# Kernel optimization log

Hardware: AMD Instinct MI355X
Metric: run time of the kernel (lower is better)

The kernel has to match this reference:

```python
import jax, jax.numpy as jnp
import numpy as np

WSCALE = 0.05  # keep ReLU MLP activations in a sane range


def setup_inputs() -> dict:
    key = jax.random.key(0)
    ks = jax.random.split(key, 9)
    B, D, H = 2048, 64, 512
    return {
        "x": jax.random.normal(ks[0], (B, D), dtype=jnp.float32),
        "W1": jax.random.normal(ks[1], (H, D), dtype=jnp.float32) * WSCALE,
        "b1": jax.random.normal(ks[2], (H,), dtype=jnp.float32) * WSCALE,
        "W2": jax.random.normal(ks[3], (H, H), dtype=jnp.float32) * WSCALE,
        "b2": jax.random.normal(ks[4], (H,), dtype=jnp.float32) * WSCALE,
        "W3": jax.random.normal(ks[5], (H, H), dtype=jnp.float32) * WSCALE,
        "b3": jax.random.normal(ks[6], (H,), dtype=jnp.float32) * WSCALE,
        "W4": jax.random.normal(ks[7], (D, H), dtype=jnp.float32) * WSCALE,
        "b4": jax.random.normal(ks[8], (D,), dtype=jnp.float32) * WSCALE,
    }


def reference(x, W1, b1, W2, b2, W3, b3, W4, b4):
    # Score network: ReLU MLP (weights stored PyTorch-style [out, in]).
    a1 = x @ W1.T + b1          # [B, H]
    h1 = jax.nn.relu(a1)
    a2 = h1 @ W2.T + b2
    h2 = jax.nn.relu(a2)
    a3 = h2 @ W3.T + b3
    h3 = jax.nn.relu(a3)
    s = h3 @ W4.T + b4          # [B, D] score

    # Divergence = trace of Jacobian ds/dx per sample.
    # Per-sample J = W4 @ diag(m3) @ W3 @ diag(m2) @ W2 @ diag(m1) @ W1,
    # with m_k = 1[a_k > 0] (ReLU derivative; 0 at 0 like torch autograd).
    m1 = (a1 > 0).astype(x.dtype)
    m2 = (a2 > 0).astype(x.dtype)
    m3 = (a3 > 0).astype(x.dtype)
    T = m1[:, :, None] * W1[None, :, :]                 # [B, H, D]
    T = m2[:, :, None] * jnp.einsum('ij,bjd->bid', W2, T)  # [B, H, D]
    T = m3[:, :, None] * jnp.einsum('ij,bjd->bid', W3, T)  # [B, H, D]
    div = jnp.einsum('dj,bjd->b', W4, T)                # trace of J, [B]

    # Hyvarinen score: 0.5 * ||s||^2 + div
    val = 0.5 * jnp.sum(s * s, axis=1) + div
    return val
```

## Files before the change

kernel.cpp:

```cpp
#include <hip/hip_runtime.h>
#include <stdint.h>


typedef __attribute__((ext_vector_type(8))) short short8;
typedef __attribute__((ext_vector_type(4))) float f32x4;

union U16x8 {
  uint4 u;
  short8 s;
};

__device__ __forceinline__ uint16_t f2bf(float f) {
  uint32_t u = __float_as_uint(f);
  uint32_t lsb = (u >> 16) & 1u;
  u += 0x7FFFu + lsb;
  return (uint16_t)(u >> 16);
}

__device__ __forceinline__ void lds_load16(const uint4* gsrc, uint4* ldst) {
  __builtin_amdgcn_global_load_lds(
      (const __attribute__((address_space(1))) void*)gsrc,
      (__attribute__((address_space(3))) void*)ldst, 16, 0, 0);
}

__global__ __launch_bounds__(256) void convert_kernel(
    const float* __restrict__ W1, const float* __restrict__ W2,
    const float* __restrict__ W3, const float* __restrict__ W4,
    uint16_t* __restrict__ A2swz, uint16_t* __restrict__ A3swz,
    uint16_t* __restrict__ B1swz, uint16_t* __restrict__ B4swz,
    float* __restrict__ W2Tf, float* __restrict__ W3Tf,
    float* __restrict__ W1Tf, float* __restrict__ W4Tf) {
  const int i = blockIdx.x * 256 + threadIdx.x;
  if (i < 262144) {
    const int e = i;
    const int f = e >> 3, j = e & 7;
    const int lane = f & 63, fk = f >> 6;
    const int kc = fk & 15, r16 = fk >> 4;
    const int l15 = lane & 15, quad = lane >> 4;
    const int row = r16 * 16 + l15, col = kc * 32 + quad * 8 + j;
    A2swz[e] = f2bf(W2[row * 512 + col]);
  } else if (i < 524288) {
    const int e = i - 262144;
    const int f = e >> 3, j = e & 7;
    const int lane = f & 63, fk = f >> 6;
    const int kc = fk & 15, r16 = fk >> 4;
    const int l15 = lane & 15, quad = lane >> 4;
    const int row = r16 * 16 + l15, col = kc * 32 + quad * 8 + j;
    A3swz[e] = f2bf(W3[col * 512 + row]);
  } else if (i < 557056) {
    const int e = i - 524288;
    const int f = e >> 3, j = e & 7;
    const int lane = f & 63, fk = f >> 6;
    const int kc = fk >> 2, jt = fk & 3;
    const int l15 = lane & 15, quad = lane >> 4;
    const int d = jt * 16 + l15, col = kc * 32 + quad * 8 + j;
    B1swz[e] = f2bf(W1[col * 64 + d]);
  } else if (i < 589824) {
    const int e = i - 557056;
    const int f = e >> 3, j = e & 7;
    const int lane = f & 63, fk = f >> 6;
    const int kc = fk >> 2, jt = fk & 3;
    const int l15 = lane & 15, quad = lane >> 4;
    const int d = jt * 16 + l15, col = kc * 32 + quad * 8 + j;
    B4swz[e] = f2bf(W4[d * 512 + col]);
  } else if (i < 851968) {
    const int e = i - 589824;
    const int k = e >> 9, jj = e & 511;
    W2Tf[e] = W2[jj * 512 + k];
  } else if (i < 1114112) {
    const int e = i - 851968;
    const int k = e >> 9, jj = e & 511;
    W3Tf[e] = W3[jj * 512 + k];
  } else if (i < 1146880) {
    const int e = i - 1114112;
    const int k = e >> 9, jj = e & 511;
    W1Tf[e] = W1[jj * 64 + k];
  } else if (i < 1179648) {
    const int e = i - 1146880;
    const int k = e >> 6, d = e & 63;
    W4Tf[e] = W4[d * 512 + k];
  }
}

__device__ __forceinline__ void relu_store_mask4(
    float acc[4], float (*hdst)[4], uint32_t* __restrict__ mbase,
    int t, int lane, int wv) {
#pragma unroll
  for (int s = 0; s < 4; ++s) {
    const unsigned long long bal = __ballot(acc[s] > 0.f);
    if (lane == 0) {
      uint2 w2;
      w2.x = (uint32_t)bal;
      w2.y = (uint32_t)(bal >> 32);
      *(uint2*)(mbase + (size_t)s * 16 + 2 * wv) = w2;
    }
  }
  float4 r;
  r.x = acc[0] > 0.f ? acc[0] : 0.f;
  r.y = acc[1] > 0.f ? acc[1] : 0.f;
  r.z = acc[2] > 0.f ? acc[2] : 0.f;
  r.w = acc[3] > 0.f ? acc[3] : 0.f;
  *(float4*)&hdst[t][0] = r;
}

__device__ __forceinline__ void fwd_layer(
    const float* __restrict__ WT, const float* __restrict__ bias,
    const float (* __restrict__ src)[4], float (* __restrict__ dst)[4],
    uint32_t* __restrict__ mbase, int t, int lane, int wv, int K) {
  float acc[4];
  {
    const float bj = bias[t];
    acc[0] = bj; acc[1] = bj; acc[2] = bj; acc[3] = bj;
  }
  const float* Wp = WT + t;
  float wA[8], wB[8];
#pragma unroll
  for (int j = 0; j < 8; ++j) wA[j] = Wp[(size_t)j * 512];
#pragma unroll 1
  for (int kb = 0; kb < K; kb += 16) {
#pragma unroll
    for (int j = 0; j < 8; ++j) wB[j] = Wp[(size_t)(kb + 8 + j) * 512];
#pragma unroll
    for (int j = 0; j < 8; ++j) {
      const float4 h = *(const float4*)&src[kb + j][0];
      const float w = wA[j];
      acc[0] = fmaf(w, h.x, acc[0]); acc[1] = fmaf(w, h.y, acc[1]);
      acc[2] = fmaf(w, h.z, acc[2]); acc[3] = fmaf(w, h.w, acc[3]);
    }
    if (kb + 16 < K) {
#pragma unroll
      for (int j = 0; j < 8; ++j) wA[j] = Wp[(size_t)(kb + 16 + j) * 512];
    }
#pragma unroll
    for (int j = 0; j < 8; ++j) {
      const float4 h = *(const float4*)&src[kb + 8 + j][0];
      const float w = wB[j];
      acc[0] = fmaf(w, h.x, acc[0]); acc[1] = fmaf(w, h.y, acc[1]);
      acc[2] = fmaf(w, h.z, acc[2]); acc[3] = fmaf(w, h.w, acc[3]);
    }
  }
  relu_store_mask4(acc, dst, mbase, t, lane, wv);
}

__global__ __launch_bounds__(512) void forward_kernel(
    const float* __restrict__ x,
    const float* __restrict__ W1Tf, const float* __restrict__ b1,
    const float* __restrict__ W2Tf, const float* __restrict__ b2,
    const float* __restrict__ W3Tf, const float* __restrict__ b3,
    const float* __restrict__ W4Tf, const float* __restrict__ b4,
    uint32_t* __restrict__ m1p, uint32_t* __restrict__ m2p,
    uint32_t* __restrict__ m3p, float* __restrict__ out) {
  __shared__ float xs[64][4];
  __shared__ float hA[512][4];
  __shared__ float hB[512][4];
  __shared__ float p4[4][2][64];
  const int t = threadIdx.x;
  const int lane = t & 63, wv = t >> 6;
  const int b0 = blockIdx.x * 4;

  if (t < 256) {
    const int k = t >> 2, s = t & 3;
    xs[k][s] = x[(size_t)(b0 + s) * 64 + k];
  }
  __syncthreads();

  fwd_layer(W1Tf, b1, xs, hA, m1p + (size_t)b0 * 16, t, lane, wv, 64);
  __syncthreads();
  fwd_layer(W2Tf, b2, hA, hB, m2p + (size_t)b0 * 16, t, lane, wv, 512);
  __syncthreads();
  fwd_layer(W3Tf, b3, hB, hA, m3p + (size_t)b0 * 16, t, lane, wv, 512);
  __syncthreads();

  {
    const int s = wv & 3, hh = wv >> 2, d = lane;
    const int k0 = hh * 256;
    const float* Wp = W4Tf + (size_t)k0 * 64 + d;
    float ap[4] = {0.f, 0.f, 0.f, 0.f};
    float wA[8], wB[8];
#pragma unroll
    for (int j = 0; j < 8; ++j) wA[j] = Wp[(size_t)j * 64];
#pragma unroll 1
    for (int kb = 0; kb < 256; kb += 16) {
#pragma unroll
      for (int j = 0; j < 8; ++j) wB[j] = Wp[(size_t)(kb + 8 + j) * 64];
#pragma unroll
      for (int j = 0; j < 8; ++j)
        ap[j & 3] = fmaf(wA[j], hA[k0 + kb + j][s], ap[j & 3]);
      if (kb + 16 < 256) {
#pragma unroll
        for (int j = 0; j < 8; ++j) wA[j] = Wp[(size_t)(kb + 16 + j) * 64];
      }
#pragma unroll
      for (int j = 0; j < 8; ++j)
        ap[j & 3] = fmaf(wB[j], hA[k0 + kb + 8 + j][s], ap[j & 3]);
    }
    p4[s][hh][d] = (ap[0] + ap[1]) + (ap[2] + ap[3]);
  }
  __syncthreads();
  if (wv < 4) {
    const int s = wv, d = lane;
    const float a4 = p4[s][0][d] + p4[s][1][d] + b4[d];
    float sq = a4 * a4;
#pragma unroll
    for (int off = 32; off; off >>= 1) sq += __shfl_down(sq, off, 64);
    if (lane == 0) out[b0 + s] = 0.5f * sq;
  }
}

__device__ __forceinline__ void expand_mask(uint32_t byte8, uint32_t mk[4]) {
#pragma unroll
  for (int i = 0; i < 4; ++i) {
    mk[i] = (((byte8 >> (2 * i)) & 1u) ? 0x0000FFFFu : 0u) |
            (((byte8 >> (2 * i + 1)) & 1u) ? 0xFFFF0000u : 0u);
  }
}

__global__ __launch_bounds__(512, 4) void div_kernel(
    const uint4* __restrict__ A2swz, const uint4* __restrict__ A3swz,
    const uint4* __restrict__ B1swz, const uint4* __restrict__ B4swz,
    const uint32_t* __restrict__ m1p, const uint32_t* __restrict__ m2p,
    const uint32_t* __restrict__ m3p, float* __restrict__ out) {
  __shared__ uint4 sfrag[3][16][64];
  __shared__ uint4 emask[8][16][4];
  const int t = threadIdx.x;
  const int lane = t & 63, wv = t >> 6;
  const int quad = lane >> 4, l15 = lane & 15;
  const int g4 = blockIdx.x;
  const int rowB0 = blockIdx.y * 64;
  const int sLoc = wv & 3;
  const int b = g4 * 4 + sLoc;
  const int r16b = blockIdx.y * 4;
  const bool isC = (wv < 4);

  const uint4* sb = (wv < 2) ? A2swz : (wv < 4) ? B1swz : (wv < 6) ? A3swz : B4swz;

  f32x4 acc[4][4];
#pragma unroll
  for (int it = 0; it < 4; ++it)
#pragma unroll
    for (int jt = 0; jt < 4; ++jt) acc[it][jt] = (f32x4){0.f, 0.f, 0.f, 0.f};

  {
    const uint32_t* mp = (isC ? m1p : m3p) + (size_t)b * 16;
    const int kcl = lane >> 2, qd = lane & 3;
    const uint32_t word = mp[kcl];
    uint32_t mk[4];
    expand_mask((word >> (qd * 8)) & 0xFFu, mk);
    uint4 v;
    v.x = mk[0]; v.y = mk[1]; v.z = mk[2]; v.w = mk[3];
    emask[wv][kcl][qd] = v;
  }

  auto stage = [&](int sbuf, int kc) {
#pragma unroll
    for (int q = 0; q < 2; ++q) {
      const int sub = (wv & 1) * 2 + q;
      const size_t off = ((wv & 2) == 0)
          ? ((size_t)((r16b + sub) * 16 + kc) * 64 + lane)
          : ((size_t)(kc * 4 + sub) * 64 + lane);
      lds_load16(sb + off, &sfrag[sbuf][wv * 2 + q][0]);
    }
  };

  stage(0, 0);
  stage(1, 1);
  __builtin_amdgcn_sched_barrier(0);
  asm volatile("s_waitcnt vmcnt(2)" ::: "memory");
  __builtin_amdgcn_s_barrier();
  __builtin_amdgcn_sched_barrier(0);

  const int base = isC ? 0 : 8;

#pragma unroll 1
  for (int kc = 0; kc < 16; ++kc) {
    const int rb = kc % 3;
    if (kc < 14) stage((kc + 2) % 3, kc + 2);

    const uint4 mku = emask[wv][kc][quad];

    uint4 a[4], u[4];
#pragma unroll
    for (int q = 0; q < 4; ++q) {
      a[q] = sfrag[rb][base + q][lane];
      u[q] = sfrag[rb][base + 4 + q][lane];
    }

    short8 bf[4];
#pragma unroll
    for (int jt = 0; jt < 4; ++jt) {
      U16x8 uu;
      uu.u = u[jt];
      uu.u.x &= mku.x; uu.u.y &= mku.y; uu.u.z &= mku.z; uu.u.w &= mku.w;
      bf[jt] = uu.s;
    }
#pragma unroll
    for (int it = 0; it < 4; ++it) {
      U16x8 ua;
      ua.u = a[it];
      const short8 af = ua.s;
#pragma unroll
      for (int jt = 0; jt < 4; ++jt)
        acc[it][jt] = __builtin_amdgcn_mfma_f32_16x16x32_bf16(af, bf[jt], acc[it][jt], 0, 0, 0);
    }

    if (kc < 14) {
      asm volatile("s_waitcnt vmcnt(2)" ::: "memory");
    } else if (kc == 14) {
      asm volatile("s_waitcnt vmcnt(0)" ::: "memory");
    }
    if (kc < 15) {
      __builtin_amdgcn_s_barrier();
      __builtin_amdgcn_sched_barrier(0);
    }
  }

  __syncthreads();
  float* cxf = (float*)&sfrag[0][0][0];
  float dsum = 0.f;
  const uint32_t* m2w = m2p + (size_t)b * 16;
#pragma unroll
  for (int h = 0; h < 2; ++h) {
    if (isC) {
#pragma unroll
      for (int ith = 0; ith < 2; ++ith)
#pragma unroll
        for (int jt = 0; jt < 4; ++jt) {
          float* crow = &cxf[((size_t)sLoc * 32 + ith * 16 + quad * 4) * 65 +
                             jt * 16 + l15];
          crow[0 * 65] = acc[h * 2 + ith][jt][0];
          crow[1 * 65] = acc[h * 2 + ith][jt][1];
          crow[2 * 65] = acc[h * 2 + ith][jt][2];
          crow[3 * 65] = acc[h * 2 + ith][jt][3];
        }
    }
    __syncthreads();
    if (!isC) {
#pragma unroll
      for (int ith = 0; ith < 2; ++ith) {
        const int it = h * 2 + ith;
        const int rloc = it * 16 + quad * 4;
        const uint32_t md = m2w[(rowB0 + rloc) >> 5];
        const uint32_t bits = (md >> (rloc & 31)) & 0xFu;
        const float w0 = (bits & 1u) ? 1.f : 0.f;
        const float w1 = (bits & 2u) ? 1.f : 0.f;
        const float w2 = (bits & 4u) ? 1.f : 0.f;
        const float w3 = (bits & 8u) ? 1.f : 0.f;
#pragma unroll
        for (int jt = 0; jt < 4; ++jt) {
          const float* crow = &cxf[((size_t)sLoc * 32 + ith * 16 + quad * 4) * 65 +
                                   jt * 16 + l15];
          dsum = fmaf(w0, acc[it][jt][0] * crow[0 * 65], dsum);
          dsum = fmaf(w1, acc[it][jt][1] * crow[1 * 65], dsum);
          dsum = fmaf(w2, acc[it][jt][2] * crow[2 * 65], dsum);
          dsum = fmaf(w3, acc[it][jt][3] * crow[3 * 65], dsum);
        }
      }
    }
    __syncthreads();
  }
  if (!isC) {
#pragma unroll
    for (int off = 32; off; off >>= 1) dsum += __shfl_down(dsum, off, 64);
    if (lane == 0) atomicAdd(out + b, dsum);
  }
}

extern "C" void kernel_launch(void* const* d_in, const int* in_sizes, int n_in,
                              void* d_out, int out_size, void* d_ws, size_t ws_size,
                              hipStream_t stream) {
  const float* x  = (const float*)d_in[0];
  const float* W1 = (const float*)d_in[1];
  const float* b1 = (const float*)d_in[2];
  const float* W2 = (const float*)d_in[3];
  const float* b2 = (const float*)d_in[4];
  const float* W3 = (const float*)d_in[5];
  const float* b3 = (const float*)d_in[6];
  const float* W4 = (const float*)d_in[7];
  const float* b4 = (const float*)d_in[8];
  float* out = (float*)d_out;

  char* ws = (char*)d_ws;
  uint16_t* A2swz = (uint16_t*)(ws + 0);
  uint16_t* A3swz = (uint16_t*)(ws + 524288);
  uint16_t* B1swz = (uint16_t*)(ws + 1048576);
  uint16_t* B4swz = (uint16_t*)(ws + 1114112);
  float*    W2Tf  = (float*)(ws + 1179648);
  float*    W3Tf  = (float*)(ws + 2228224);
  float*    W1Tf  = (float*)(ws + 3276800);
  float*    W4Tf  = (float*)(ws + 3407872);
  uint32_t* m1p   = (uint32_t*)(ws + 3538944);
  uint32_t* m2p   = (uint32_t*)(ws + 3670016);
  uint32_t* m3p   = (uint32_t*)(ws + 3801088);
  if (ws_size < 3932160) return;

  convert_kernel<<<4608, 256, 0, stream>>>(W1, W2, W3, W4,
                                           A2swz, A3swz, B1swz, B4swz,
                                           W2Tf, W3Tf, W1Tf, W4Tf);
  forward_kernel<<<512, 512, 0, stream>>>(x, W1Tf, b1, W2Tf, b2, W3Tf, b3,
                                          W4Tf, b4, m1p, m2p, m3p, out);
  div_kernel<<<dim3(512, 8), 512, 0, stream>>>((const uint4*)A2swz,
                                               (const uint4*)A3swz,
                                               (const uint4*)B1swz,
                                               (const uint4*)B4swz,
                                               m1p, m2p, m3p, out);
}
```

Before: 266.0 us.

## Load masked B fragments straight to registers, stage only A through LDS

Each wave now loads its B operand fragments (B1 or B4) from global memory directly into registers, prefetched one k-chunk ahead. Only the A operand (A2 or A3) still goes through the triple-buffered LDS ring, with one async load per wave instead of two. This halves the per-iteration LDS reads and shrinks the async staging work. In exchange, each wave fetches B on its own rather than sharing it through LDS, which adds redundant global/L2 traffic and register pressure. The vmcnt waits are adjusted to match the new number of outstanding loads.

Result: slower. 271.7 us (+2.1%).

```diff
diff --git a/kernel.cpp b/kernel.cpp
--- a/kernel.cpp
+++ b/kernel.cpp
@@ -232,7 +232,8 @@
   const int r16b = blockIdx.y * 4;
   const bool isC = (wv < 4);
 
-  const uint4* sb = (wv < 2) ? A2swz : (wv < 4) ? B1swz : (wv < 6) ? A3swz : B4swz;
+  const uint4* sbA = isC ? A2swz : A3swz;
+  const uint4* sbB = isC ? B1swz : B4swz;
 
   f32x4 acc[4][4];
 #pragma unroll
@@ -251,48 +252,48 @@
     emask[wv][kcl][qd] = v;
   }
 
-  auto stage = [&](int sbuf, int kc) {
-#pragma unroll
-    for (int q = 0; q < 2; ++q) {
-      const int sub = (wv & 1) * 2 + q;
-      const size_t off = ((wv & 2) == 0)
-          ? ((size_t)((r16b + sub) * 16 + kc) * 64 + lane)
-          : ((size_t)(kc * 4 + sub) * 64 + lane);
-      lds_load16(sb + off, &sfrag[sbuf][wv * 2 + q][0]);
-    }
+  auto stageA = [&](int sbuf, int kc) {
+    const size_t off = (size_t)((r16b + (wv & 3)) * 16 + kc) * 64 + lane;
+    lds_load16(sbA + off, &sfrag[sbuf][wv][0]);
   };
 
-  stage(0, 0);
-  stage(1, 1);
+  uint4 bfr[4];
+  stageA(0, 0);
+#pragma unroll
+  for (int jt = 0; jt < 4; ++jt) bfr[jt] = sbB[(size_t)jt * 64 + lane];
+  stageA(1, 1);
   __builtin_amdgcn_sched_barrier(0);
-  asm volatile("s_waitcnt vmcnt(2)" ::: "memory");
+  asm volatile("s_waitcnt vmcnt(1)" ::: "memory");
   __builtin_amdgcn_s_barrier();
   __builtin_amdgcn_sched_barrier(0);
 
-  const int base = isC ? 0 : 8;
+  const int base = isC ? 0 : 4;
 
 #pragma unroll 1
   for (int kc = 0; kc < 16; ++kc) {
     const int rb = kc % 3;
-    if (kc < 14) stage((kc + 2) % 3, kc + 2);
 
     const uint4 mku = emask[wv][kc][quad];
-
-    uint4 a[4], u[4];
-#pragma unroll
-    for (int q = 0; q < 4; ++q) {
-      a[q] = sfrag[rb][base + q][lane];
-      u[q] = sfrag[rb][base + 4 + q][lane];
-    }
 
     short8 bf[4];
 #pragma unroll
     for (int jt = 0; jt < 4; ++jt) {
       U16x8 uu;
-      uu.u = u[jt];
+      uu.u = bfr[jt];
       uu.u.x &= mku.x; uu.u.y &= mku.y; uu.u.z &= mku.z; uu.u.w &= mku.w;
       bf[jt] = uu.s;
     }
+    if (kc < 15) {
+#pragma unroll
+      for (int jt = 0; jt < 4; ++jt)
+        bfr[jt] = sbB[(size_t)((kc + 1) * 4 + jt) * 64 + lane];
+    }
+    if (kc < 14) stageA((kc + 2) % 3, kc + 2);
+
+    uint4 a[4];
+#pragma unroll
+    for (int q = 0; q < 4; ++q) a[q] = sfrag[rb][base + q][lane];
+
 #pragma unroll
     for (int it = 0; it < 4; ++it) {
       U16x8 ua;
@@ -304,7 +305,7 @@
     }
 
     if (kc < 14) {
-      asm volatile("s_waitcnt vmcnt(2)" ::: "memory");
+      asm volatile("s_waitcnt vmcnt(1)" ::: "memory");
     } else if (kc == 14) {
       asm volatile("s_waitcnt vmcnt(0)" ::: "memory");
     }
```

## Repartition divergence kernel waves by row tile instead of sample

Applied to the files above, without the earlier changes.

Each wave now owns one 16-row A tile and loops over the 4 samples in the block, applying each sample's mask to the A fragment instead of the B fragment. Before, each wave handled one sample and loaded all 4 A tiles. This cuts per-wave LDS reads of A fragments from 4 to 1 per k-step while keeping the MFMA count the same. The cost is 4 mask reads and ANDs per step, plus 4 reductions and 4 atomics per wave at the end. The first barrier now also waits for LDS counter zero so the mask table is visible.

Result: slower. 273.4 us (+2.8%).

```diff
diff --git a/kernel.cpp b/kernel.cpp
--- a/kernel.cpp
+++ b/kernel.cpp
@@ -221,86 +221,88 @@
     const uint32_t* __restrict__ m1p, const uint32_t* __restrict__ m2p,
     const uint32_t* __restrict__ m3p, float* __restrict__ out) {
   __shared__ uint4 sfrag[3][16][64];
-  __shared__ uint4 emask[8][16][4];
+  __shared__ uint4 emask2[2][4][16][4];
   const int t = threadIdx.x;
   const int lane = t & 63, wv = t >> 6;
   const int quad = lane >> 4, l15 = lane & 15;
   const int g4 = blockIdx.x;
   const int rowB0 = blockIdx.y * 64;
-  const int sLoc = wv & 3;
-  const int b = g4 * 4 + sLoc;
+  const int q = wv & 3;
   const int r16b = blockIdx.y * 4;
   const bool isC = (wv < 4);
+  const int role = isC ? 0 : 1;
 
   const uint4* sb = (wv < 2) ? A2swz : (wv < 4) ? B1swz : (wv < 6) ? A3swz : B4swz;
 
   f32x4 acc[4][4];
 #pragma unroll
-  for (int it = 0; it < 4; ++it)
-#pragma unroll
-    for (int jt = 0; jt < 4; ++jt) acc[it][jt] = (f32x4){0.f, 0.f, 0.f, 0.f};
+  for (int s = 0; s < 4; ++s)
+#pragma unroll
+    for (int jt = 0; jt < 4; ++jt) acc[s][jt] = (f32x4){0.f, 0.f, 0.f, 0.f};
 
   {
-    const uint32_t* mp = (isC ? m1p : m3p) + (size_t)b * 16;
+    const int r = wv >> 2, s = wv & 3;
+    const uint32_t* mp = (r == 0 ? m1p : m3p) + (size_t)(g4 * 4 + s) * 16;
     const int kcl = lane >> 2, qd = lane & 3;
     const uint32_t word = mp[kcl];
     uint32_t mk[4];
     expand_mask((word >> (qd * 8)) & 0xFFu, mk);
     uint4 v;
     v.x = mk[0]; v.y = mk[1]; v.z = mk[2]; v.w = mk[3];
-    emask[wv][kcl][qd] = v;
+    emask2[r][s][kcl][qd] = v;
   }
 
   auto stage = [&](int sbuf, int kc) {
 #pragma unroll
-    for (int q = 0; q < 2; ++q) {
-      const int sub = (wv & 1) * 2 + q;
+    for (int qq = 0; qq < 2; ++qq) {
+      const int sub = (wv & 1) * 2 + qq;
       const size_t off = ((wv & 2) == 0)
           ? ((size_t)((r16b + sub) * 16 + kc) * 64 + lane)
           : ((size_t)(kc * 4 + sub) * 64 + lane);
-      lds_load16(sb + off, &sfrag[sbuf][wv * 2 + q][0]);
+      lds_load16(sb + off, &sfrag[sbuf][wv * 2 + qq][0]);
     }
   };
 
   stage(0, 0);
   stage(1, 1);
   __builtin_amdgcn_sched_barrier(0);
-  asm volatile("s_waitcnt vmcnt(2)" ::: "memory");
+  asm volatile("s_waitcnt vmcnt(2) lgkmcnt(0)" ::: "memory");
   __builtin_amdgcn_s_barrier();
   __builtin_amdgcn_sched_barrier(0);
 
-  const int base = isC ? 0 : 8;
+  const int abase = isC ? 0 : 8;
+  const int ubase = isC ? 4 : 12;
 
 #pragma unroll 1
   for (int kc = 0; kc < 16; ++kc) {
     const int rb = kc % 3;
     if (kc < 14) stage((kc + 2) % 3, kc + 2);
 
-    const uint4 mku = emask[wv][kc][quad];
-
-    uint4 a[4], u[4];
-#pragma unroll
-    for (int q = 0; q < 4; ++q) {
-      a[q] = sfrag[rb][base + q][lane];
-      u[q] = sfrag[rb][base + 4 + q][lane];
-    }
-
-    short8 bf[4];
+    const uint4 a1 = sfrag[rb][abase + q][lane];
+    uint4 u[4];
+#pragma unroll
+    for (int jt = 0; jt < 4; ++jt) u[jt] = sfrag[rb][ubase + jt][lane];
+
+    short8 bu[4];
 #pragma unroll
     for (int jt = 0; jt < 4; ++jt) {
       U16x8 uu;
       uu.u = u[jt];
-      uu.u.x &= mku.x; uu.u.y &= mku.y; uu.u.z &= mku.z; uu.u.w &= mku.w;
-      bf[jt] = uu.s;
-    }
-#pragma unroll
-    for (int it = 0; it < 4; ++it) {
-      U16x8 ua;
-      ua.u = a[it];
-      const short8 af = ua.s;
+      bu[jt] = uu.s;
+    }
+
+#pragma unroll
+    for (int s = 0; s < 4; ++s) {
+      const uint4 mku = emask2[role][s][kc][quad];
+      U16x8 am;
+      am.u.x = a1.x & mku.x;
+      am.u.y = a1.y & mku.y;
+      am.u.z = a1.z & mku.z;
+      am.u.w = a1.w & mku.w;
+      const short8 af = am.s;
 #pragma unroll
       for (int jt = 0; jt < 4; ++jt)
-        acc[it][jt] = __builtin_amdgcn_mfma_f32_16x16x32_bf16(af, bf[jt], acc[it][jt], 0, 0, 0);
+        acc[s][jt] = __builtin_amdgcn_mfma_f32_16x16x32_bf16(af, bu[jt], acc[s][jt], 0, 0, 0);
     }
 
     if (kc < 14) {
@@ -316,29 +318,31 @@
 
   __syncthreads();
   float* cxf = (float*)&sfrag[0][0][0];
-  float dsum = 0.f;
-  const uint32_t* m2w = m2p + (size_t)b * 16;
+  float dsum[4] = {0.f, 0.f, 0.f, 0.f};
 #pragma unroll
   for (int h = 0; h < 2; ++h) {
     if (isC) {
 #pragma unroll
-      for (int ith = 0; ith < 2; ++ith)
+      for (int sh = 0; sh < 2; ++sh) {
+        const int s = h * 2 + sh;
 #pragma unroll
         for (int jt = 0; jt < 4; ++jt) {
-          float* crow = &cxf[((size_t)sLoc * 32 + ith * 16 + quad * 4) * 65 +
+          float* crow = &cxf[((size_t)(q * 2 + sh) * 16 + quad * 4) * 65 +
                              jt * 16 + l15];
-          crow[0 * 65] = acc[h * 2 + ith][jt][0];
-          crow[1 * 65] = acc[h * 2 + ith][jt][1];
-          crow[2 * 65] = acc[h * 2 + ith][jt][2];
-          crow[3 * 65] = acc[h * 2 + ith][jt][3];
+          crow[0 * 65] = acc[s][jt][0];
+          crow[1 * 65] = acc[s][jt][1];
+          crow[2 * 65] = acc[s][jt][2];
+          crow[3 * 65] = acc[s][jt][3];
         }
+      }
     }
     __syncthreads();
     if (!isC) {
 #pragma unroll
-      for (int ith = 0; ith < 2; ++ith) {
-        const int it = h * 2 + ith;
-        const int rloc = it * 16 + quad * 4;
+      for (int sh = 0; sh < 2; ++sh) {
+        const int s = h * 2 + sh;
+        const uint32_t* m2w = m2p + (size_t)(g4 * 4 + s) * 16;
+        const int rloc = q * 16 + quad * 4;
         const uint32_t md = m2w[(rowB0 + rloc) >> 5];
         const uint32_t bits = (md >> (rloc & 31)) & 0xFu;
         const float w0 = (bits & 1u) ? 1.f : 0.f;
@@ -347,12 +351,12 @@
         const float w3 = (bits & 8u) ? 1.f : 0.f;
 #pragma unroll
         for (int jt = 0; jt < 4; ++jt) {
-          const float* crow = &cxf[((size_t)sLoc * 32 + ith * 16 + quad * 4) * 65 +
+          const float* crow = &cxf[((size_t)(q * 2 + sh) * 16 + quad * 4) * 65 +
                                    jt * 16 + l15];
-          dsum = fmaf(w0, acc[it][jt][0] * crow[0 * 65], dsum);
-          dsum = fmaf(w1, acc[it][jt][1] * crow[1 * 65], dsum);
-          dsum = fmaf(w2, acc[it][jt][2] * crow[2 * 65], dsum);
-          dsum = fmaf(w3, acc[it][jt][3] * crow[3 * 65], dsum);
+          dsum[s] = fmaf(w0, acc[s][jt][0] * crow[0 * 65], dsum[s]);
+          dsum[s] = fmaf(w1, acc[s][jt][1] * crow[1 * 65], dsum[s]);
+          dsum[s] = fmaf(w2, acc[s][jt][2] * crow[2 * 65], dsum[s]);
+          dsum[s] = fmaf(w3, acc[s][jt][3] * crow[3 * 65], dsum[s]);
         }
       }
     }
@@ -360,8 +364,12 @@
   }
   if (!isC) {
 #pragma unroll
-    for (int off = 32; off; off >>= 1) dsum += __shfl_down(dsum, off, 64);
-    if (lane == 0) atomicAdd(out + b, dsum);
+    for (int s = 0; s < 4; ++s) {
+      float v = dsum[s];
+#pragma unroll
+      for (int off = 32; off; off >>= 1) v += __shfl_down(v, off, 64);
+      if (lane == 0) atomicAdd(out + (g4 * 4 + s), v);
+    }
   }
 }
 
```

## Restructure forward MLP to split-K with 8 outputs per thread and 256 threads

Applied to the files above, without the earlier changes.

The forward kernel now runs 256 threads per block. Each wave takes a quarter of the K dimension and each thread accumulates 8 output neurons across 4 samples, so every LDS activation load is reused across 8 weights. Partial sums are reduced through a shared buffer, followed by bias, mask ballots and ReLU. The intent is to cut LDS traffic per FMA and raise ILP, at the cost of extra shared memory, a reduction step and more barriers. The output layer uses the same split-K layout.

After: 264.4 us. No clear change (-0.6%).

```diff
diff --git a/kernel.cpp b/kernel.cpp
--- a/kernel.cpp
+++ b/kernel.cpp
@@ -82,67 +82,92 @@
   }
 }
 
-__device__ __forceinline__ void relu_store_mask4(
-    float acc[4], float (*hdst)[4], uint32_t* __restrict__ mbase,
-    int t, int lane, int wv) {
-#pragma unroll
-  for (int s = 0; s < 4; ++s) {
-    const unsigned long long bal = __ballot(acc[s] > 0.f);
-    if (lane == 0) {
-      uint2 w2;
-      w2.x = (uint32_t)bal;
-      w2.y = (uint32_t)(bal >> 32);
-      *(uint2*)(mbase + (size_t)s * 16 + 2 * wv) = w2;
-    }
-  }
+__device__ __forceinline__ float4 frelu4(float a0, float a1, float a2, float a3) {
   float4 r;
-  r.x = acc[0] > 0.f ? acc[0] : 0.f;
-  r.y = acc[1] > 0.f ? acc[1] : 0.f;
-  r.z = acc[2] > 0.f ? acc[2] : 0.f;
-  r.w = acc[3] > 0.f ? acc[3] : 0.f;
-  *(float4*)&hdst[t][0] = r;
-}
-
-__device__ __forceinline__ void fwd_layer(
+  r.x = a0 > 0.f ? a0 : 0.f;
+  r.y = a1 > 0.f ? a1 : 0.f;
+  r.z = a2 > 0.f ? a2 : 0.f;
+  r.w = a3 > 0.f ? a3 : 0.f;
+  return r;
+}
+
+template <int KPW>
+__device__ __forceinline__ void fwd_layer8(
     const float* __restrict__ WT, const float* __restrict__ bias,
-    const float (* __restrict__ src)[4], float (* __restrict__ dst)[4],
-    uint32_t* __restrict__ mbase, int t, int lane, int wv, int K) {
-  float acc[4];
-  {
-    const float bj = bias[t];
-    acc[0] = bj; acc[1] = bj; acc[2] = bj; acc[3] = bj;
-  }
-  const float* Wp = WT + t;
+    const float4* __restrict__ src, float4* __restrict__ dst,
+    float4 (* __restrict__ pa)[512], uint32_t* __restrict__ mbase,
+    int t, int lane, int kh) {
+  float acc[8][4];
+#pragma unroll
+  for (int p = 0; p < 8; ++p)
+#pragma unroll
+    for (int s = 0; s < 4; ++s) acc[p][s] = 0.f;
+
+  const int k0 = kh * KPW;
+  const float* Wb = WT + (size_t)k0 * 512 + lane;
   float wA[8], wB[8];
 #pragma unroll
-  for (int j = 0; j < 8; ++j) wA[j] = Wp[(size_t)j * 512];
+  for (int p = 0; p < 8; ++p) wA[p] = Wb[p * 64];
+  float4 hA_ = src[k0];
+
 #pragma unroll 1
-  for (int kb = 0; kb < K; kb += 16) {
-#pragma unroll
-    for (int j = 0; j < 8; ++j) wB[j] = Wp[(size_t)(kb + 8 + j) * 512];
-#pragma unroll
-    for (int j = 0; j < 8; ++j) {
-      const float4 h = *(const float4*)&src[kb + j][0];
-      const float w = wA[j];
-      acc[0] = fmaf(w, h.x, acc[0]); acc[1] = fmaf(w, h.y, acc[1]);
-      acc[2] = fmaf(w, h.z, acc[2]); acc[3] = fmaf(w, h.w, acc[3]);
-    }
-    if (kb + 16 < K) {
-#pragma unroll
-      for (int j = 0; j < 8; ++j) wA[j] = Wp[(size_t)(kb + 16 + j) * 512];
-    }
-#pragma unroll
-    for (int j = 0; j < 8; ++j) {
-      const float4 h = *(const float4*)&src[kb + 8 + j][0];
-      const float w = wB[j];
-      acc[0] = fmaf(w, h.x, acc[0]); acc[1] = fmaf(w, h.y, acc[1]);
-      acc[2] = fmaf(w, h.z, acc[2]); acc[3] = fmaf(w, h.w, acc[3]);
-    }
-  }
-  relu_store_mask4(acc, dst, mbase, t, lane, wv);
-}
-
-__global__ __launch_bounds__(512) void forward_kernel(
+  for (int kk = 0; kk < KPW; kk += 2) {
+    const float4 hB_ = src[k0 + kk + 1];
+#pragma unroll
+    for (int p = 0; p < 8; ++p) wB[p] = Wb[(size_t)(kk + 1) * 512 + p * 64];
+#pragma unroll
+    for (int p = 0; p < 8; ++p) {
+      acc[p][0] = fmaf(wA[p], hA_.x, acc[p][0]);
+      acc[p][1] = fmaf(wA[p], hA_.y, acc[p][1]);
+      acc[p][2] = fmaf(wA[p], hA_.z, acc[p][2]);
+      acc[p][3] = fmaf(wA[p], hA_.w, acc[p][3]);
+    }
+    hA_ = src[k0 + kk + 2];
+#pragma unroll
+    for (int p = 0; p < 8; ++p) wA[p] = Wb[(size_t)(kk + 2) * 512 + p * 64];
+#pragma unroll
+    for (int p = 0; p < 8; ++p) {
+      acc[p][0] = fmaf(wB[p], hB_.x, acc[p][0]);
+      acc[p][1] = fmaf(wB[p], hB_.y, acc[p][1]);
+      acc[p][2] = fmaf(wB[p], hB_.z, acc[p][2]);
+      acc[p][3] = fmaf(wB[p], hB_.w, acc[p][3]);
+    }
+  }
+
+#pragma unroll
+  for (int p = 0; p < 8; ++p) {
+    float4 v;
+    v.x = acc[p][0]; v.y = acc[p][1]; v.z = acc[p][2]; v.w = acc[p][3];
+    pa[kh][p * 64 + lane] = v;
+  }
+  __syncthreads();
+
+#pragma unroll
+  for (int pass = 0; pass < 2; ++pass) {
+    const int u = pass * 256 + t;
+    const float4 a0 = pa[0][u], a1 = pa[1][u], a2 = pa[2][u], a3 = pa[3][u];
+    const float bj = bias[u];
+    float a[4];
+    a[0] = ((a0.x + a1.x) + (a2.x + a3.x)) + bj;
+    a[1] = ((a0.y + a1.y) + (a2.y + a3.y)) + bj;
+    a[2] = ((a0.z + a1.z) + (a2.z + a3.z)) + bj;
+    a[3] = ((a0.w + a1.w) + (a2.w + a3.w)) + bj;
+#pragma unroll
+    for (int s = 0; s < 4; ++s) {
+      const unsigned long long bal = __ballot(a[s] > 0.f);
+      if (lane == 0) {
+        uint2 w2;
+        w2.x = (uint32_t)bal;
+        w2.y = (uint32_t)(bal >> 32);
+        *(uint2*)(mbase + (size_t)s * 16 + pass * 8 + 2 * kh) = w2;
+      }
+    }
+    dst[u] = frelu4(a[0], a[1], a[2], a[3]);
+  }
+  __syncthreads();
+}
+
+__global__ __launch_bounds__(256) void forward_kernel(
     const float* __restrict__ x,
     const float* __restrict__ W1Tf, const float* __restrict__ b1,
     const float* __restrict__ W2Tf, const float* __restrict__ b2,
@@ -150,60 +175,70 @@
     const float* __restrict__ W4Tf, const float* __restrict__ b4,
     uint32_t* __restrict__ m1p, uint32_t* __restrict__ m2p,
     uint32_t* __restrict__ m3p, float* __restrict__ out) {
-  __shared__ float xs[64][4];
-  __shared__ float hA[512][4];
-  __shared__ float hB[512][4];
-  __shared__ float p4[4][2][64];
+  __shared__ float4 xs[64];
+  __shared__ float4 hU[512];
+  __shared__ float4 hV[512];
+  __shared__ float4 pa[4][512];
   const int t = threadIdx.x;
-  const int lane = t & 63, wv = t >> 6;
+  const int lane = t & 63, kh = t >> 6;
   const int b0 = blockIdx.x * 4;
 
-  if (t < 256) {
-    const int k = t >> 2, s = t & 3;
-    xs[k][s] = x[(size_t)(b0 + s) * 64 + k];
+  {
+    const int k2 = t >> 2, s2 = t & 3;
+    ((float*)&xs[k2])[s2] = x[(size_t)(b0 + s2) * 64 + k2];
   }
   __syncthreads();
 
-  fwd_layer(W1Tf, b1, xs, hA, m1p + (size_t)b0 * 16, t, lane, wv, 64);
+  fwd_layer8<16>(W1Tf, b1, xs, hU, pa, m1p + (size_t)b0 * 16, t, lane, kh);
+  fwd_layer8<128>(W2Tf, b2, hU, hV, pa, m2p + (size_t)b0 * 16, t, lane, kh);
+  fwd_layer8<128>(W3Tf, b3, hV, hU, pa, m3p + (size_t)b0 * 16, t, lane, kh);
+
+  {
+    const int d = lane;
+    const int k0 = kh * 128;
+    const float* Wb = W4Tf + (size_t)k0 * 64 + d;
+    float a4[4] = {0.f, 0.f, 0.f, 0.f};
+    float wA = Wb[0], wB;
+    float4 hA_ = hU[k0], hB_;
+#pragma unroll 1
+    for (int kk = 0; kk < 128; kk += 2) {
+      hB_ = hU[k0 + kk + 1];
+      wB = Wb[(size_t)(kk + 1) * 64];
+      a4[0] = fmaf(wA, hA_.x, a4[0]); a4[1] = fmaf(wA, hA_.y, a4[1]);
+      a4[2] = fmaf(wA, hA_.z, a4[2]); a4[3] = fmaf(wA, hA_.w, a4[3]);
+      hA_ = hU[k0 + kk + 2];
+      wA = Wb[(size_t)(kk + 2) * 64];
+      a4[0] = fmaf(wB, hB_.x, a4[0]); a4[1] = fmaf(wB, hB_.y, a4[1]);
+      a4[2] = fmaf(wB, hB_.z, a4[2]); a4[3] = fmaf(wB, hB_.w, a4[3]);
+    }
+    float4 v;
+    v.x = a4[0]; v.y = a4[1]; v.z = a4[2]; v.w = a4[3];
+    pa[kh][d] = v;
+  }
   __syncthreads();
-  fwd_layer(W2Tf, b2, hA, hB, m2p + (size_t)b0 * 16, t, lane, wv, 512);
-  __syncthreads();
-  fwd_layer(W3Tf, b3, hB, hA, m3p + (size_t)b0 * 16, t, lane, wv, 512);
-  __syncthreads();
-
-  {
-    const int s = wv & 3, hh = wv >> 2, d = lane;
-    const int k0 = hh * 256;
-    const float* Wp = W4Tf + (size_t)k0 * 64 + d;
-    float ap[4] = {0.f, 0.f, 0.f, 0.f};
-    float wA[8], wB[8];
-#pragma unroll
-    for (int j = 0; j < 8; ++j) wA[j] = Wp[(size_t)j * 64];
-#pragma unroll 1
-    for (int kb = 0; kb < 256; kb += 16) {
-#pragma unroll
-      for (int j = 0; j < 8; ++j) wB[j] = Wp[(size_t)(kb + 8 + j) * 64];
-#pragma unroll
-      for (int j = 0; j < 8; ++j)
-        ap[j & 3] = fmaf(wA[j], hA[k0 + kb + j][s], ap[j & 3]);
-      if (kb + 16 < 256) {
-#pragma unroll
-        for (int j = 0; j < 8; ++j) wA[j] = Wp[(size_t)(kb + 16 + j) * 64];
-      }
-#pragma unroll
-      for (int j = 0; j < 8; ++j)
-        ap[j & 3] = fmaf(wB[j], hA[k0 + kb + 8 + j][s], ap[j & 3]);
-    }
-    p4[s][hh][d] = (ap[0] + ap[1]) + (ap[2] + ap[3]);
-  }
-  __syncthreads();
-  if (wv < 4) {
-    const int s = wv, d = lane;
-    const float a4 = p4[s][0][d] + p4[s][1][d] + b4[d];
-    float sq = a4 * a4;
-#pragma unroll
-    for (int off = 32; off; off >>= 1) sq += __shfl_down(sq, off, 64);
-    if (lane == 0) out[b0 + s] = 0.5f * sq;
+  if (t < 64) {
+    const float4 q0 = pa[0][t], q1 = pa[1][t], q2 = pa[2][t], q3 = pa[3][t];
+    const float bj = b4[t];
+    float sq[4];
+    sq[0] = ((q0.x + q1.x) + (q2.x + q3.x)) + bj;
+    sq[1] = ((q0.y + q1.y) + (q2.y + q3.y)) + bj;
+    sq[2] = ((q0.z + q1.z) + (q2.z + q3.z)) + bj;
+    sq[3] = ((q0.w + q1.w) + (q2.w + q3.w)) + bj;
+#pragma unroll
+    for (int s = 0; s < 4; ++s) sq[s] *= sq[s];
+#pragma unroll
+    for (int off = 32; off; off >>= 1) {
+      sq[0] += __shfl_down(sq[0], off, 64);
+      sq[1] += __shfl_down(sq[1], off, 64);
+      sq[2] += __shfl_down(sq[2], off, 64);
+      sq[3] += __shfl_down(sq[3], off, 64);
+    }
+    if (t == 0) {
+      out[b0 + 0] = 0.5f * sq[0];
+      out[b0 + 1] = 0.5f * sq[1];
+      out[b0 + 2] = 0.5f * sq[2];
+      out[b0 + 3] = 0.5f * sq[3];
+    }
   }
 }
 
@@ -396,7 +431,7 @@
   convert_kernel<<<4608, 256, 0, stream>>>(W1, W2, W3, W4,
                                            A2swz, A3swz, B1swz, B4swz,
                                            W2Tf, W3Tf, W1Tf, W4Tf);
-  forward_kernel<<<512, 512, 0, stream>>>(x, W1Tf, b1, W2Tf, b2, W3Tf, b3,
+  forward_kernel<<<512, 256, 0, stream>>>(x, W1Tf, b1, W2Tf, b2, W3Tf, b3,
                                           W4Tf, b4, m1p, m2p, m3p, out);
   div_kernel<<<dim3(512, 8), 512, 0, stream>>>((const uint4*)A2swz,
                                                (const uint4*)A3swz,
```
